# Optimization experiments

Hardware: AMD Instinct MI355X
Metric: run time of the kernel (lower is better)

## Reference

```python
import jax, jax.numpy as jnp
from jax import lax
import numpy as np

B, T = 512, 20
RES, C3D, AUD, P, H, NC = 2048, 4096, 128, 1024, 1024, 200


def setup_inputs() -> dict:
    key = jax.random.key(0)
    ks = jax.random.split(key, 40)

    def n(k, shape, s=0.02):
        return jax.random.normal(k, shape, jnp.float32) * s

    inp = {
        "resnet_features": jax.random.normal(ks[0], (B, T, RES), jnp.float32),
        "c3d_features": jax.random.normal(ks[1], (B, T, C3D), jnp.float32),
        "audio_features": jax.random.normal(ks[2], (B, T, AUD), jnp.float32),
        "W_audio": n(ks[3], (P, AUD)), "b_audio": jnp.zeros((P,), jnp.float32),
        "W_resnet": n(ks[4], (P, RES)), "b_resnet": jnp.zeros((P,), jnp.float32),
        "W_c3d": n(ks[5], (P, C3D)), "b_c3d": jnp.zeros((P,), jnp.float32),
    }
    i = 6
    for nm in ["audio_fwd", "audio_rev", "resnet_fwd", "resnet_rev", "c3d_fwd", "c3d_rev"]:
        inp[nm + "_Wih"] = n(ks[i], (4 * H, P)); i += 1
        inp[nm + "_Whh"] = n(ks[i], (4 * H, H)); i += 1
        inp[nm + "_bih"] = jnp.zeros((4 * H,), jnp.float32)
        inp[nm + "_bhh"] = jnp.zeros((4 * H,), jnp.float32)
    inp["W_out"] = n(ks[i], (NC, 2 * H)); i += 1
    inp["b_out"] = jnp.zeros((NC,), jnp.float32)
    return inp


def _run_lstm(xs, Wih, Whh, bih, bhh, reverse):
    # xs: (B, T, P). PyTorch LSTMCell gate order: i, f, g, o.
    b = bih + bhh

    def step(carry, x):
        h, c = carry
        gates = x @ Wih.T + h @ Whh.T + b  # (B, 4H)
        i, f, g, o = jnp.split(gates, 4, axis=-1)
        c = jax.nn.sigmoid(f) * c + jax.nn.sigmoid(i) * jnp.tanh(g)
        h = jax.nn.sigmoid(o) * jnp.tanh(c)
        return (h, c), None

    bsz = xs.shape[0]
    init = (jnp.zeros((bsz, H), xs.dtype), jnp.zeros((bsz, H), xs.dtype))
    (h, c), _ = lax.scan(step, init, jnp.swapaxes(xs, 0, 1), reverse=reverse)
    return h


def reference(resnet_features, c3d_features, audio_features, W_audio, b_audio, W_resnet, b_resnet, W_c3d, b_c3d, audio_fwd_Wih, audio_fwd_Whh, audio_fwd_bih, audio_fwd_bhh, audio_rev_Wih, audio_rev_Whh, audio_rev_bih, audio_rev_bhh, resnet_fwd_Wih, resnet_fwd_Whh, resnet_fwd_bih, resnet_fwd_bhh, resnet_rev_Wih, resnet_rev_Whh, resnet_rev_bih, resnet_rev_bhh, c3d_fwd_Wih, c3d_fwd_Whh, c3d_fwd_bih, c3d_fwd_bhh, c3d_rev_Wih, c3d_rev_Whh, c3d_rev_bih, c3d_rev_bhh, W_out, b_out):
    # Dropouts are identity in eval mode.
    out_a = audio_features @ W_audio.T + b_audio    # (B, T, P)
    out_r = resnet_features @ W_resnet.T + b_resnet
    out_c = c3d_features @ W_c3d.T + b_c3d

    h_af = _run_lstm(out_a, audio_fwd_Wih, audio_fwd_Whh, audio_fwd_bih, audio_fwd_bhh, False)
    h_ar = _run_lstm(out_a, audio_rev_Wih, audio_rev_Whh, audio_rev_bih, audio_rev_bhh, True)
    h_rf = _run_lstm(out_r, resnet_fwd_Wih, resnet_fwd_Whh, resnet_fwd_bih, resnet_fwd_bhh, False)
    h_rr = _run_lstm(out_r, resnet_rev_Wih, resnet_rev_Whh, resnet_rev_bih, resnet_rev_bhh, True)
    h_cf = _run_lstm(out_c, c3d_fwd_Wih, c3d_fwd_Whh, c3d_fwd_bih, c3d_fwd_bhh, False)
    h_cr = _run_lstm(out_c, c3d_rev_Wih, c3d_rev_Whh, c3d_rev_bih, c3d_rev_bhh, True)

    audio_final = jnp.concatenate([h_af, h_ar], axis=1)
    resnet_final = jnp.concatenate([h_rf, h_rr], axis=1)
    c3d_final = jnp.concatenate([h_cf, h_cr], axis=1)
    fused = audio_final * resnet_final * c3d_final  # (B, 2H)
    return fused @ W_out.T + b_out  # (B, NC)
```

## Files before the change

kernel.cpp:

```cpp
#include <hip/hip_runtime.h>
#include <cstdio>
#include <cstdint>

#define TT    20
#define BATCH 512
#define HID   1024
#define G4    4096
#define NG    8192
#define BT    (BATCH * TT)
#define NCLS  200
#define SH    ((size_t)BATCH * HID)

typedef unsigned short u16;
typedef __attribute__((ext_vector_type(8))) short short8;
typedef __attribute__((ext_vector_type(4))) float f32x4;
typedef __attribute__((ext_vector_type(4))) unsigned short u16x4;

__device__ __forceinline__ float sigf(float x) { return 1.0f / (1.0f + __expf(-x)); }

__device__ __forceinline__ u16 f2bf(float x) {
    unsigned u = __float_as_uint(x);
    u += 0x7FFFu + ((u >> 16) & 1u);
    return (u16)(u >> 16);
}
__device__ __forceinline__ float bf2f(u16 b) { return __uint_as_float(((unsigned)b) << 16); }

__device__ __forceinline__ void gld16(const u16* g, u16* l) {
    __builtin_amdgcn_global_load_lds(
        (const __attribute__((address_space(1))) void*)g,
        (__attribute__((address_space(3))) void*)l, 16, 0, 0);
}

__global__ void cvt4_kernel(const float* __restrict__ x, u16* __restrict__ y, int n4)
{
    const int stride = gridDim.x * blockDim.x;
    for (int i = blockIdx.x * blockDim.x + threadIdx.x; i < n4; i += stride) {
        const float4 v = ((const float4*)x)[i];
        uint2 hp;
        hp.x = (unsigned)f2bf(v.x) | ((unsigned)f2bf(v.y) << 16);
        hp.y = (unsigned)f2bf(v.z) | ((unsigned)f2bf(v.w) << 16);
        ((uint2*)y)[i] = hp;
    }
}

__global__ void bias_cat_kernel(const float* __restrict__ bi0, const float* __restrict__ bh0,
                                const float* __restrict__ bi1, const float* __restrict__ bh1,
                                float* __restrict__ bcat)
{
    const int n = blockIdx.x * blockDim.x + threadIdx.x;
    if (n >= NG) return;
    bcat[n] = (n < G4) ? (bi0[n] + bh0[n]) : (bi1[n - G4] + bh1[n - G4]);
}

template<int MODE>
__launch_bounds__(256)
__global__ void gemm_b16(const u16* __restrict__ A, const u16* __restrict__ W,
                         const float* __restrict__ b1, u16* __restrict__ Cb,
                         int M, int N, int K, int cm)
{
    __shared__ u16 sA[4][128][8]; __shared__ u16 sW[4][128][8];
    const int tid = threadIdx.x, lane = tid & 63, w = tid >> 6;
    const int wr = w >> 1, wc = w & 1;

    const int nwg = gridDim.x;
    const int cpx = nwg >> 3;
    const int lg = (blockIdx.x & 7) * cpx + (blockIdx.x >> 3);
    const int nby = N >> 7;
    const int cb = cm * nby;
    const int chunk = lg / cb;
    const int r = lg - chunk * cb;
    const int m0 = (chunk * cm + (r % cm)) * 128;
    const int n0 = (r / cm) * 128;

    const u16* A0 = A + (size_t)m0 * K;
    const u16* W0 = W + (size_t)n0 * K;

    f32x4 acc[4][4];
#pragma unroll
    for (int i = 0; i < 4; ++i)
#pragma unroll
        for (int j = 0; j < 4; ++j) acc[i][j] = f32x4{0.f, 0.f, 0.f, 0.f};

    const int u1 = tid, u2 = tid + 256;
    const size_t go1 = (size_t)(u1 & 127) * K + (u1 >> 7) * 8;
    const size_t go2 = (size_t)(u2 & 127) * K + (u2 >> 7) * 8;
    u16* const l1 = (u16*)sA + (size_t)u1 * 8;
    u16* const l2 = (u16*)sA + (size_t)u2 * 8;
    const size_t dW = (u16*)sW - (u16*)sA;

    for (int k0 = 0; k0 < K; k0 += 32) {
        gld16(A0 + go1 + k0, l1);       gld16(A0 + go2 + k0, l2);
        gld16(W0 + go1 + k0, l1 + dW);  gld16(W0 + go2 + k0, l2 + dW);
        __syncthreads();

        const int kb = lane >> 4, rr = lane & 15;
        short8 Av[4], Wv[4];
#pragma unroll
        for (int i = 0; i < 4; ++i) {
            Av[i] = *(const short8*)&sA[kb][wr * 64 + i * 16 + rr][0];
            Wv[i] = *(const short8*)&sW[kb][wc * 64 + i * 16 + rr][0];
        }
#pragma unroll
        for (int i = 0; i < 4; ++i)
#pragma unroll
            for (int j = 0; j < 4; ++j)
                acc[i][j] = __builtin_amdgcn_mfma_f32_16x16x32_bf16(Av[i], Wv[j], acc[i][j], 0, 0, 0);
        __syncthreads();
    }

    const int rr = lane & 15, rg = lane >> 4;
#pragma unroll
    for (int j = 0; j < 4; ++j) {
        const int col = n0 + wc * 64 + j * 16 + rr;
        const float bias = b1 ? b1[col] : 0.f;
#pragma unroll
        for (int i = 0; i < 4; ++i) {
            if (MODE == 1) {
                u16x4 pk;
#pragma unroll
                for (int q = 0; q < 4; ++q) pk[q] = f2bf(acc[i][j][q] + bias);
                const int grp = (m0 >> 2) + wr * 16 + i * 4 + rg;
                __builtin_nontemporal_store(pk, (u16x4*)(Cb + ((size_t)grp * N + col) * 4));
            } else {
#pragma unroll
                for (int q = 0; q < 4; ++q) {
                    const int row = m0 + wr * 64 + i * 16 + rg * 4 + q;
                    const int rowp = (row % 20) * 512 + row / 20;
                    Cb[(size_t)rowp * N + col] = f2bf(acc[i][j][q] + bias);
                }
            }
        }
    }
}

__launch_bounds__(256)
__global__ void lstm_step6(const u16* __restrict__ whhAll,
                           const u16* __restrict__ Gall,
                           const u16* __restrict__ hinAll,
                           u16* __restrict__ houtAll,
                           float* __restrict__ cbAll,
                           float* __restrict__ hfinAll,
                           int s, int write_hfin)
{
    const int l = blockIdx.z;
    __shared__ u16 sA[2][4][64][8];
    __shared__ u16 sW[2][4][128][8];
    const int tid = threadIdx.x, lane = tid & 63, w = tid >> 6;
    const int wr = w >> 1, wc = w & 1;
    const int j0 = blockIdx.x * 32;
    const int m0 = blockIdx.y * 64;

    const u16* __restrict__ hin = hinAll + (size_t)l * SH;
    const u16* __restrict__ Whh = whhAll + (size_t)l * G4 * HID;
    const int do_gemm = (s > 0);

    f32x4 acc[2][4];
#pragma unroll
    for (int i = 0; i < 2; ++i)
#pragma unroll
        for (int g = 0; g < 4; ++g) acc[i][g] = f32x4{0.f, 0.f, 0.f, 0.f};

    const int rr = lane & 15, rg = lane >> 4;

    if (do_gemm) {
        const size_t goA = (size_t)(m0 + (tid & 63)) * HID + (tid >> 6) * 8;
        const int rW = tid & 127;
        const int wrow = ((rW >> 4) & 3) * HID + j0 + (rW >> 6) * 16 + (rW & 15);
        const size_t goW1 = (size_t)wrow * HID + (tid >> 7) * 8;
        const size_t goW2 = (size_t)wrow * HID + ((tid >> 7) + 2) * 8;
        u16* const ldA  = (u16*)sA + (size_t)tid * 8;
        u16* const ldW1 = (u16*)sW + (size_t)tid * 8;
        u16* const ldW2 = (u16*)sW + (size_t)(tid + 256) * 8;

        gld16(hin + goA,  ldA);
        gld16(Whh + goW1, ldW1);
        gld16(Whh + goW2, ldW2);
        __syncthreads();

        for (int k0 = 0; k0 < HID; k0 += 32) {
            const int bf = (k0 >> 5) & 1;
            if (k0 + 32 < HID) {
                gld16(hin + goA  + k0 + 32, ldA  + (bf ^ 1) * 2048);
                gld16(Whh + goW1 + k0 + 32, ldW1 + (bf ^ 1) * 4096);
                gld16(Whh + goW2 + k0 + 32, ldW2 + (bf ^ 1) * 4096);
            }
            const int kb = lane >> 4;
            short8 Av[2], Wv[4];
#pragma unroll
            for (int i = 0; i < 2; ++i)
                Av[i] = *(const short8*)&sA[bf][kb][wr * 32 + i * 16 + rr][0];
#pragma unroll
            for (int g = 0; g < 4; ++g)
                Wv[g] = *(const short8*)&sW[bf][kb][wc * 64 + g * 16 + rr][0];
#pragma unroll
            for (int i = 0; i < 2; ++i)
#pragma unroll
                for (int g = 0; g < 4; ++g)
                    acc[i][g] = __builtin_amdgcn_mfma_f32_16x16x32_bf16(Av[i], Wv[g], acc[i][g], 0, 0, 0);
            __syncthreads();
        }
    }

    const int j = j0 + wc * 16 + rr;
    const int t = (l & 1) ? (TT - 1 - s) : s;
    const u16* __restrict__ Gl = Gall + (size_t)(l >> 1) * BT * NG;
    const int cbase = (l & 1) * G4 + j;
    float* __restrict__ cb = cbAll + (size_t)l * SH;
    float* __restrict__ hf = hfinAll + (size_t)l * SH;
    u16* __restrict__ ho = houtAll + (size_t)l * SH;
#pragma unroll
    for (int i = 0; i < 2; ++i) {
        const int grp = t * 128 + (m0 >> 2) + wr * 8 + i * 4 + rg;
        const u16* gb = Gl + (size_t)grp * NG * 4;
        const u16x4 g0 = __builtin_nontemporal_load((const u16x4*)(gb + (size_t)cbase * 4));
        const u16x4 g1 = __builtin_nontemporal_load((const u16x4*)(gb + (size_t)(cbase + 1024) * 4));
        const u16x4 g2 = __builtin_nontemporal_load((const u16x4*)(gb + (size_t)(cbase + 2048) * 4));
        const u16x4 g3 = __builtin_nontemporal_load((const u16x4*)(gb + (size_t)(cbase + 3072) * 4));
#pragma unroll
        for (int q = 0; q < 4; ++q) {
            const int b = m0 + wr * 32 + i * 16 + rg * 4 + q;
            const float pi = acc[i][0][q] + bf2f(g0[q]);
            const float pf = acc[i][1][q] + bf2f(g1[q]);
            const float pg = acc[i][2][q] + bf2f(g2[q]);
            const float po = acc[i][3][q] + bf2f(g3[q]);
            const size_t idx = (size_t)b * HID + j;
            const float cprev = do_gemm ? cb[idx] : 0.f;
            const float cn = sigf(pf) * cprev + sigf(pi) * tanhf(pg);
            cb[idx] = cn;
            const float h = sigf(po) * tanhf(cn);
            if (write_hfin) hf[idx] = h;
            else            ho[idx] = f2bf(h);
        }
    }
}

__global__ void fuse_mul_kernel(const float* __restrict__ hfin, float* __restrict__ fused)
{
    const int idx = blockIdx.x * blockDim.x + threadIdx.x;
    if (idx >= BATCH * 2 * HID) return;
    const int b = idx >> 11;
    const int n = idx & 2047;
    const int half = n >> 10;
    const int j = n & 1023;
    const size_t o = (size_t)b * HID + j;
    fused[idx] = hfin[(size_t)(0 + half) * SH + o] *
                 hfin[(size_t)(2 + half) * SH + o] *
                 hfin[(size_t)(4 + half) * SH + o];
}

__launch_bounds__(256)
__global__ void gemm_bias_kernel(const float* __restrict__ A, const float* __restrict__ W,
                                 const float* __restrict__ b1,
                                 float* __restrict__ C, int M, int N, int K)
{
    __shared__ float As[16][68];
    __shared__ float Ws[16][68];
    const int tid = threadIdx.x;
    const int tx = tid & 15, ty = tid >> 4;
    const int m0 = blockIdx.x * 64;
    const int n0 = blockIdx.y * 64;
    const int lr = tid >> 2;
    const int lk = (tid & 3) << 2;
    const bool mok = (m0 + lr < M);
    const bool nok = (n0 + lr < N);
    const float* Arow = A + (size_t)(m0 + lr) * K + lk;
    const float* Wrow = W + (size_t)(n0 + lr) * K + lk;
    float acc[4][4] = {};

    for (int k0 = 0; k0 < K; k0 += 16) {
        float4 av = make_float4(0.f, 0.f, 0.f, 0.f);
        float4 wv = make_float4(0.f, 0.f, 0.f, 0.f);
        if (mok) av = *(const float4*)(Arow + k0);
        if (nok) wv = *(const float4*)(Wrow + k0);
        As[lk + 0][lr] = av.x; As[lk + 1][lr] = av.y; As[lk + 2][lr] = av.z; As[lk + 3][lr] = av.w;
        Ws[lk + 0][lr] = wv.x; Ws[lk + 1][lr] = wv.y; Ws[lk + 2][lr] = wv.z; Ws[lk + 3][lr] = wv.w;
        __syncthreads();
#pragma unroll
        for (int k = 0; k < 16; ++k) {
            const float4 a = *(const float4*)&As[k][ty << 2];
            const float4 ww = *(const float4*)&Ws[k][tx << 2];
            const float a4[4] = {a.x, a.y, a.z, a.w};
            const float w4[4] = {ww.x, ww.y, ww.z, ww.w};
#pragma unroll
            for (int i = 0; i < 4; ++i)
#pragma unroll
                for (int j = 0; j < 4; ++j)
                    acc[i][j] = fmaf(a4[i], w4[j], acc[i][j]);
        }
        __syncthreads();
    }

#pragma unroll
    for (int i = 0; i < 4; ++i) {
        const int m = m0 + (ty << 2) + i;
        if (m >= M) continue;
#pragma unroll
        for (int j = 0; j < 4; ++j) {
            const int n = n0 + (tx << 2) + j;
            if (n >= N) continue;
            C[(size_t)m * N + n] = acc[i][j] + (b1 ? b1[n] : 0.f);
        }
    }
}

extern "C" void kernel_launch(void* const* d_in, const int* in_sizes, int n_in,
                              void* d_out, int out_size, void* d_ws, size_t ws_size,
                              hipStream_t stream)
{
    const float* resnet   = (const float*)d_in[0];
    const float* c3d      = (const float*)d_in[1];
    const float* audio    = (const float*)d_in[2];
    const float* W_audio  = (const float*)d_in[3];
    const float* b_audio  = (const float*)d_in[4];
    const float* W_resnet = (const float*)d_in[5];
    const float* b_resnet = (const float*)d_in[6];
    const float* W_c3d    = (const float*)d_in[7];
    const float* b_c3d    = (const float*)d_in[8];
    const float* Wih[6]; const float* Whh[6]; const float* bih[6]; const float* bhh[6];
    for (int l = 0; l < 6; ++l) {
        Wih[l] = (const float*)d_in[9 + 4 * l];
        Whh[l] = (const float*)d_in[10 + 4 * l];
        bih[l] = (const float*)d_in[11 + 4 * l];
        bhh[l] = (const float*)d_in[12 + 4 * l];
    }
    const float* W_out = (const float*)d_in[33];
    const float* b_out = (const float*)d_in[34];
    float* out = (float*)d_out;

    const float* feat[3] = { audio, resnet, c3d };
    const float* fw[3]   = { W_audio, W_resnet, W_c3d };
    const float* fb[3]   = { b_audio, b_resnet, b_c3d };
    const int    fK[3]   = { 128, 2048, 4096 };

    char* p = (char*)d_ws;
    char* pend = p + ws_size;
    auto alloc = [&](size_t bytes) -> void* {
        void* q = p; p += (bytes + 255) & ~(size_t)255; return q;
    };
    const size_t FW = (size_t)1024 * (128 + 2048 + 4096);
    u16* Gall  = (u16*)alloc((size_t)3 * BT * NG * 2);
    u16* featB = Gall + (size_t)2 * BT * NG;
    u16* fwB   = (u16*)alloc(FW * 2);
    u16* wihB  = (u16*)alloc((size_t)NG * HID * 2);
    u16* whhB  = (u16*)alloc((size_t)3 * NG * HID * 2);
    u16* projB = (u16*)alloc((size_t)BT * HID * 2);
    float* bcat = (float*)alloc((size_t)NG * 4);
    u16* hA    = (u16*)alloc((size_t)6 * SH * 2);
    u16* hB    = (u16*)alloc((size_t)6 * SH * 2);
    float* cb    = (float*)alloc((size_t)6 * SH * 4);
    float* hfin  = (float*)alloc((size_t)6 * SH * 4);
    float* fused = (float*)alloc((size_t)BATCH * 2 * HID * 4);
    if (p > pend) {
        fprintf(stderr, "kernel_launch: ws too small: need %zu have %zu\n",
                (size_t)(p - (char*)d_ws), ws_size);
        return;
    }

    const dim3 blk(256);
    const size_t fwOff[3] = { 0, (size_t)1024 * 128, (size_t)1024 * 128 + (size_t)1024 * 2048 };

    for (int st = 0; st < 3; ++st) {
        const int n4 = (1024 * fK[st]) / 4;
        cvt4_kernel<<<dim3(min(2048, (n4 + 255) / 256)), blk, 0, stream>>>(
            fw[st], fwB + fwOff[st], n4);
    }

    for (int st = 0; st < 3; ++st) {
        const int K = fK[st];
        cvt4_kernel<<<dim3(2048), blk, 0, stream>>>(feat[st], featB, (BT * K) / 4);
        gemm_b16<0><<<dim3((BT / 128) * (HID / 128)), blk, 0, stream>>>(
            featB, fwB + fwOff[st], fb[st], projB, BT, HID, K, 8);
        for (int d = 0; d < 2; ++d) {
            const int l = st * 2 + d;
            cvt4_kernel<<<dim3(2048), blk, 0, stream>>>(
                Wih[l], wihB + (size_t)d * G4 * HID, (G4 * HID) / 4);
            cvt4_kernel<<<dim3(2048), blk, 0, stream>>>(
                Whh[l], whhB + (size_t)l * G4 * HID, (G4 * HID) / 4);
        }
        bias_cat_kernel<<<dim3(NG / 256), blk, 0, stream>>>(
            bih[st * 2], bhh[st * 2], bih[st * 2 + 1], bhh[st * 2 + 1], bcat);
        gemm_b16<1><<<dim3((BT / 128) * (NG / 128)), blk, 0, stream>>>(
            projB, wihB, bcat, Gall + (size_t)st * BT * NG, BT, NG, HID, 8);
    }

    for (int s = 0; s < TT; ++s) {
        const u16* in = (s & 1) ? hB : hA;
        u16*      o  = (s & 1) ? hA : hB;
        lstm_step6<<<dim3(HID / 32, BATCH / 64, 6), blk, 0, stream>>>(
            whhB, Gall, in, o, cb, hfin, s, s == TT - 1 ? 1 : 0);
    }

    fuse_mul_kernel<<<dim3((BATCH * 2 * HID) / 256), blk, 0, stream>>>(hfin, fused);

    gemm_bias_kernel<<<dim3(BATCH / 64, (NCLS + 63) / 64), blk, 0, stream>>>(
        fused, W_out, b_out, out, BATCH, NCLS, 2 * HID);
}
```

Before: 3.315 ms.

## Widen LSTM step tile to 64 hidden columns and batch weight conversions

The recurrent step kernel now computes 64 hidden units per block instead of 32. This doubles the W_hh tile in LDS and the accumulators per wave, so each loaded h tile is reused across twice as many MFMAs, and the grid shrinks from 32x8x6 to 16x8x6 blocks. Separately, the per-layer fp32-to-bf16 conversions of Whh and Wih are merged into batched launches using a job table indexed by blockIdx.y, cutting launch count. The cost is more registers and LDS per block and fewer blocks (768) to fill the device.

```diff
diff --git a/kernel.cpp b/kernel.cpp
--- a/kernel.cpp
+++ b/kernel.cpp
@@ -33,6 +33,22 @@
 
 __global__ void cvt4_kernel(const float* __restrict__ x, u16* __restrict__ y, int n4)
 {
+    const int stride = gridDim.x * blockDim.x;
+    for (int i = blockIdx.x * blockDim.x + threadIdx.x; i < n4; i += stride) {
+        const float4 v = ((const float4*)x)[i];
+        uint2 hp;
+        hp.x = (unsigned)f2bf(v.x) | ((unsigned)f2bf(v.y) << 16);
+        hp.y = (unsigned)f2bf(v.z) | ((unsigned)f2bf(v.w) << 16);
+        ((uint2*)y)[i] = hp;
+    }
+}
+
+struct CvtJob { const float* src; u16* dst; };
+struct CvtBatch { CvtJob j[6]; };
+__global__ void cvt4_batch(CvtBatch cb, int n4)
+{
+    const float* __restrict__ x = cb.j[blockIdx.y].src;
+    u16* __restrict__ y = cb.j[blockIdx.y].dst;
     const int stride = gridDim.x * blockDim.x;
     for (int i = blockIdx.x * blockDim.x + threadIdx.x; i < n4; i += stride) {
         const float4 v = ((const float4*)x)[i];
@@ -144,67 +160,67 @@
 {
     const int l = blockIdx.z;
     __shared__ u16 sA[2][4][64][8];
-    __shared__ u16 sW[2][4][128][8];
+    __shared__ u16 sW[2][4][256][8];
     const int tid = threadIdx.x, lane = tid & 63, w = tid >> 6;
     const int wr = w >> 1, wc = w & 1;
-    const int j0 = blockIdx.x * 32;
+    const int j0 = blockIdx.x * 64;
     const int m0 = blockIdx.y * 64;
 
     const u16* __restrict__ hin = hinAll + (size_t)l * SH;
     const u16* __restrict__ Whh = whhAll + (size_t)l * G4 * HID;
     const int do_gemm = (s > 0);
 
-    f32x4 acc[2][4];
+    f32x4 acc[2][2][4];
 #pragma unroll
     for (int i = 0; i < 2; ++i)
 #pragma unroll
-        for (int g = 0; g < 4; ++g) acc[i][g] = f32x4{0.f, 0.f, 0.f, 0.f};
+        for (int c = 0; c < 2; ++c)
+#pragma unroll
+            for (int g = 0; g < 4; ++g) acc[i][c][g] = f32x4{0.f, 0.f, 0.f, 0.f};
 
     const int rr = lane & 15, rg = lane >> 4;
 
     if (do_gemm) {
         const size_t goA = (size_t)(m0 + (tid & 63)) * HID + (tid >> 6) * 8;
-        const int rW = tid & 127;
-        const int wrow = ((rW >> 4) & 3) * HID + j0 + (rW >> 6) * 16 + (rW & 15);
-        const size_t goW1 = (size_t)wrow * HID + (tid >> 7) * 8;
-        const size_t goW2 = (size_t)wrow * HID + ((tid >> 7) + 2) * 8;
-        u16* const ldA  = (u16*)sA + (size_t)tid * 8;
-        u16* const ldW1 = (u16*)sW + (size_t)tid * 8;
-        u16* const ldW2 = (u16*)sW + (size_t)(tid + 256) * 8;
-
-        gld16(hin + goA,  ldA);
-        gld16(Whh + goW1, ldW1);
-        gld16(Whh + goW2, ldW2);
+        const int wrow = ((tid >> 4) & 3) * HID + j0 + (tid >> 6) * 16 + (tid & 15);
+        const size_t goW = (size_t)wrow * HID;
+        u16* const ldA = (u16*)sA + (size_t)tid * 8;
+        u16* const ldW = (u16*)sW + (size_t)tid * 8;
+
+        gld16(hin + goA, ldA);
+#pragma unroll
+        for (int c = 0; c < 4; ++c)
+            gld16(Whh + goW + c * 8, ldW + c * 2048);
         __syncthreads();
 
         for (int k0 = 0; k0 < HID; k0 += 32) {
             const int bf = (k0 >> 5) & 1;
             if (k0 + 32 < HID) {
-                gld16(hin + goA  + k0 + 32, ldA  + (bf ^ 1) * 2048);
-                gld16(Whh + goW1 + k0 + 32, ldW1 + (bf ^ 1) * 4096);
-                gld16(Whh + goW2 + k0 + 32, ldW2 + (bf ^ 1) * 4096);
+                gld16(hin + goA + k0 + 32, ldA + (bf ^ 1) * 2048);
+#pragma unroll
+                for (int c = 0; c < 4; ++c)
+                    gld16(Whh + goW + c * 8 + k0 + 32, ldW + (bf ^ 1) * 8192 + c * 2048);
             }
             const int kb = lane >> 4;
-            short8 Av[2], Wv[4];
+            short8 Av[2], Wv[8];
 #pragma unroll
             for (int i = 0; i < 2; ++i)
                 Av[i] = *(const short8*)&sA[bf][kb][wr * 32 + i * 16 + rr][0];
 #pragma unroll
-            for (int g = 0; g < 4; ++g)
-                Wv[g] = *(const short8*)&sW[bf][kb][wc * 64 + g * 16 + rr][0];
+            for (int f = 0; f < 8; ++f)
+                Wv[f] = *(const short8*)&sW[bf][kb][wc * 128 + f * 16 + rr][0];
 #pragma unroll
             for (int i = 0; i < 2; ++i)
 #pragma unroll
-                for (int g = 0; g < 4; ++g)
-                    acc[i][g] = __builtin_amdgcn_mfma_f32_16x16x32_bf16(Av[i], Wv[g], acc[i][g], 0, 0, 0);
+                for (int f = 0; f < 8; ++f)
+                    acc[i][f >> 2][f & 3] =
+                        __builtin_amdgcn_mfma_f32_16x16x32_bf16(Av[i], Wv[f], acc[i][f >> 2][f & 3], 0, 0, 0);
             __syncthreads();
         }
     }
 
-    const int j = j0 + wc * 16 + rr;
     const int t = (l & 1) ? (TT - 1 - s) : s;
     const u16* __restrict__ Gl = Gall + (size_t)(l >> 1) * BT * NG;
-    const int cbase = (l & 1) * G4 + j;
     float* __restrict__ cb = cbAll + (size_t)l * SH;
     float* __restrict__ hf = hfinAll + (size_t)l * SH;
     u16* __restrict__ ho = houtAll + (size_t)l * SH;
@@ -212,24 +228,29 @@
     for (int i = 0; i < 2; ++i) {
         const int grp = t * 128 + (m0 >> 2) + wr * 8 + i * 4 + rg;
         const u16* gb = Gl + (size_t)grp * NG * 4;
-        const u16x4 g0 = __builtin_nontemporal_load((const u16x4*)(gb + (size_t)cbase * 4));
-        const u16x4 g1 = __builtin_nontemporal_load((const u16x4*)(gb + (size_t)(cbase + 1024) * 4));
-        const u16x4 g2 = __builtin_nontemporal_load((const u16x4*)(gb + (size_t)(cbase + 2048) * 4));
-        const u16x4 g3 = __builtin_nontemporal_load((const u16x4*)(gb + (size_t)(cbase + 3072) * 4));
-#pragma unroll
-        for (int q = 0; q < 4; ++q) {
-            const int b = m0 + wr * 32 + i * 16 + rg * 4 + q;
-            const float pi = acc[i][0][q] + bf2f(g0[q]);
-            const float pf = acc[i][1][q] + bf2f(g1[q]);
-            const float pg = acc[i][2][q] + bf2f(g2[q]);
-            const float po = acc[i][3][q] + bf2f(g3[q]);
-            const size_t idx = (size_t)b * HID + j;
-            const float cprev = do_gemm ? cb[idx] : 0.f;
-            const float cn = sigf(pf) * cprev + sigf(pi) * tanhf(pg);
-            cb[idx] = cn;
-            const float h = sigf(po) * tanhf(cn);
-            if (write_hfin) hf[idx] = h;
-            else            ho[idx] = f2bf(h);
+#pragma unroll
+        for (int cg = 0; cg < 2; ++cg) {
+            const int j = j0 + (wc * 2 + cg) * 16 + rr;
+            const int cbase = (l & 1) * G4 + j;
+            const u16x4 g0 = __builtin_nontemporal_load((const u16x4*)(gb + (size_t)cbase * 4));
+            const u16x4 g1 = __builtin_nontemporal_load((const u16x4*)(gb + (size_t)(cbase + 1024) * 4));
+            const u16x4 g2 = __builtin_nontemporal_load((const u16x4*)(gb + (size_t)(cbase + 2048) * 4));
+            const u16x4 g3 = __builtin_nontemporal_load((const u16x4*)(gb + (size_t)(cbase + 3072) * 4));
+#pragma unroll
+            for (int q = 0; q < 4; ++q) {
+                const int b = m0 + wr * 32 + i * 16 + rg * 4 + q;
+                const float pi = acc[i][cg][0][q] + bf2f(g0[q]);
+                const float pf = acc[i][cg][1][q] + bf2f(g1[q]);
+                const float pg = acc[i][cg][2][q] + bf2f(g2[q]);
+                const float po = acc[i][cg][3][q] + bf2f(g3[q]);
+                const size_t idx = (size_t)b * HID + j;
+                const float cprev = do_gemm ? cb[idx] : 0.f;
+                const float cn = sigf(pf) * cprev + sigf(pi) * tanhf(pg);
+                cb[idx] = cn;
+                const float h = sigf(po) * tanhf(cn);
+                if (write_hfin) hf[idx] = h;
+                else            ho[idx] = f2bf(h);
+            }
         }
     }
 }
@@ -358,11 +379,17 @@
 
     const dim3 blk(256);
     const size_t fwOff[3] = { 0, (size_t)1024 * 128, (size_t)1024 * 128 + (size_t)1024 * 2048 };
+    const int n4w = (G4 * HID) / 4;
 
     for (int st = 0; st < 3; ++st) {
         const int n4 = (1024 * fK[st]) / 4;
         cvt4_kernel<<<dim3(min(2048, (n4 + 255) / 256)), blk, 0, stream>>>(
             fw[st], fwB + fwOff[st], n4);
+    }
+    {
+        CvtBatch b6;
+        for (int l = 0; l < 6; ++l) { b6.j[l].src = Whh[l]; b6.j[l].dst = whhB + (size_t)l * G4 * HID; }
+        cvt4_batch<<<dim3(768, 6), blk, 0, stream>>>(b6, n4w);
     }
 
     for (int st = 0; st < 3; ++st) {
@@ -370,12 +397,13 @@
         cvt4_kernel<<<dim3(2048), blk, 0, stream>>>(feat[st], featB, (BT * K) / 4);
         gemm_b16<0><<<dim3((BT / 128) * (HID / 128)), blk, 0, stream>>>(
             featB, fwB + fwOff[st], fb[st], projB, BT, HID, K, 8);
-        for (int d = 0; d < 2; ++d) {
-            const int l = st * 2 + d;
-            cvt4_kernel<<<dim3(2048), blk, 0, stream>>>(
-                Wih[l], wihB + (size_t)d * G4 * HID, (G4 * HID) / 4);
-            cvt4_kernel<<<dim3(2048), blk, 0, stream>>>(
-                Whh[l], whhB + (size_t)l * G4 * HID, (G4 * HID) / 4);
+        {
+            CvtBatch b2;
+            for (int d = 0; d < 2; ++d) {
+                b2.j[d].src = Wih[st * 2 + d];
+                b2.j[d].dst = wihB + (size_t)d * G4 * HID;
+            }
+            cvt4_batch<<<dim3(768, 2), blk, 0, stream>>>(b2, n4w);
         }
         bias_cat_kernel<<<dim3(NG / 256), blk, 0, stream>>>(
             bih[st * 2], bhh[st * 2], bih[st * 2 + 1], bhh[st * 2 + 1], bcat);
@@ -386,7 +414,7 @@
     for (int s = 0; s < TT; ++s) {
         const u16* in = (s & 1) ? hB : hA;
         u16*      o  = (s & 1) ? hA : hB;
-        lstm_step6<<<dim3(HID / 32, BATCH / 64, 6), blk, 0, stream>>>(
+        lstm_step6<<<dim3(HID / 64, BATCH / 64, 6), blk, 0, stream>>>(
             whhB, Gall, in, o, cb, hfin, s, s == TT - 1 ? 1 : 0);
     }
 
```

Result: slower. 3.440 ms (+3.8%).
